# Performance work log

Hardware: AMD Instinct MI355X
Metric: run time of the kernel (lower is better)

The kernel has to match this reference:

```python
import jax, jax.numpy as jnp
import numpy as np

N_NODES = 100000
N_EDGES = 1600000
N_FEAT = 128
N_HID = 128
N_LAYERS = 3
N_GRAPHS = 64
EPS0 = 0.1


def setup_inputs() -> dict:
    key = jax.random.key(0)
    ks = jax.random.split(key, 16)
    x = jax.random.normal(ks[0], (N_NODES, N_FEAT), dtype=jnp.float32)
    edge_index = jax.random.randint(ks[1], (2, N_EDGES), 0, N_NODES, dtype=jnp.int64)
    batch = jnp.sort(jax.random.randint(ks[2], (N_NODES,), 0, N_GRAPHS, dtype=jnp.int64))
    s = 1.0 / np.sqrt(N_HID)
    W_pre1 = jax.random.normal(ks[3], (N_FEAT, N_HID), dtype=jnp.float32) * s
    b_pre1 = jnp.zeros((N_HID,), dtype=jnp.float32)
    W_pre2 = jax.random.normal(ks[4], (N_HID, N_HID), dtype=jnp.float32) * s
    b_pre2 = jnp.zeros((N_HID,), dtype=jnp.float32)
    # stacked per-layer GIN MLP params: Linear -> ReLU -> Linear
    W1s = jax.random.normal(ks[5], (N_LAYERS, N_HID, N_HID), dtype=jnp.float32) * s
    b1s = jnp.zeros((N_LAYERS, N_HID), dtype=jnp.float32)
    W2s = jax.random.normal(ks[6], (N_LAYERS, N_HID, N_HID), dtype=jnp.float32) * s
    b2s = jnp.zeros((N_LAYERS, N_HID), dtype=jnp.float32)
    eps = jnp.full((N_LAYERS,), EPS0, dtype=jnp.float32)
    return {"x": x, "edge_index": edge_index, "batch": batch,
            "W_pre1": W_pre1, "b_pre1": b_pre1, "W_pre2": W_pre2, "b_pre2": b_pre2,
            "W1s": W1s, "b1s": b1s, "W2s": W2s, "b2s": b2s, "eps": eps}


def reference(x, edge_index, batch, W_pre1, b_pre1, W_pre2, b_pre2, W1s, b1s, W2s, b2s, eps):
    n_nodes = x.shape[0]
    src, dst = edge_index[0], edge_index[1]
    # pre-linear stack
    h = jax.nn.relu(x @ W_pre1 + b_pre1)
    h = jax.nn.relu(h @ W_pre2 + b_pre2)
    pooled = []
    for i in range(N_LAYERS):
        # GINConv: sum-aggregate neighbor features (gather from src, scatter-add to dst)
        agg = jax.ops.segment_sum(h[src], dst, num_segments=n_nodes)
        z = (1.0 + eps[i]) * h + agg
        # MLP update: Linear -> ReLU -> Linear
        h = jax.nn.relu(z @ W1s[i] + b1s[i]) @ W2s[i] + b2s[i]
        # global sum pool per graph
        pooled.append(jax.ops.segment_sum(h, batch, num_segments=N_GRAPHS))
    return jnp.concatenate(pooled, axis=1)  # [N_GRAPHS, N_LAYERS * N_HID]
```

## Files before the change

### kernel.cpp

```cpp
#include <hip/hip_runtime.h>

typedef float f32x4 __attribute__((ext_vector_type(4)));
typedef short s16x8 __attribute__((ext_vector_type(8)));

#define ECAP 36864

__device__ __forceinline__ ushort f2bf(float f) {
  uint u = __builtin_bit_cast(uint, f);
  u += 0x7fffu + ((u >> 16) & 1u);
  return (ushort)(u >> 16);
}
__device__ __forceinline__ float bfu_lo(uint u) { return __builtin_bit_cast(float, u << 16); }
__device__ __forceinline__ float bfu_hi(uint u) { return __builtin_bit_cast(float, u & 0xffff0000u); }

__global__ void k_prepw(const float* __restrict__ Wp1, const float* __restrict__ Wp2,
                        const float* __restrict__ W1s, const float* __restrict__ W2s,
                        ushort* __restrict__ Wf, int* __restrict__ bcur, int nbk) {
  int t = blockIdx.x * blockDim.x + threadIdx.x;
  if (t <= nbk) bcur[t] = t * ECAP;
  if (t >= 8 * 2048) return;
  int m = t >> 11;
  int r = t & 2047;
  int lane = r & 63;
  int ksnt = r >> 6;
  int ks = ksnt & 3;
  int nt = ksnt >> 2;
  const float* src = (m == 0) ? Wp1 : (m == 1) ? Wp2
                     : (m < 5) ? (W1s + (size_t)(m - 2) * 16384)
                               : (W2s + (size_t)(m - 5) * 16384);
  ushort* dst = Wf + (size_t)m * 16384 + (size_t)r * 8;
  int c = nt * 16 + (lane & 15);
  int kbase = ks * 32 + (lane >> 4) * 8;
  for (int i = 0; i < 8; ++i) dst[i] = f2bf(src[(size_t)(kbase + i) * 128 + c]);
}

#define PNBK 64
#define PCAP 80
#define PEPB 2048
__global__ __launch_bounds__(256)
void k_part(const int* __restrict__ src, const int* __restrict__ dst,
            int* __restrict__ bcur, uint2* __restrict__ ebuf, int E) {
  __shared__ uint2 stage[PNBK][PCAP];
  __shared__ int lcnt[PNBK];
  int tid = threadIdx.x;
  if (tid < PNBK) lcnt[tid] = 0;
  __syncthreads();
  int e0 = blockIdx.x * PEPB;
  for (int r = 0; r < PEPB / 256; ++r) {
    int e = e0 + r * 256 + tid;
    if (e < E) {
      int d = dst[e], s = src[e];
      int b = d >> 11;
      int pos = atomicAdd(&lcnt[b], 1);
      uint2 pr; pr.x = (uint)s; pr.y = (uint)d;
      if (pos < PCAP) {
        stage[b][pos] = pr;
      } else {
        int p = atomicAdd(&bcur[b], 1);
        ebuf[p] = pr;
      }
    }
    if (r == 3 || r == PEPB / 256 - 1) {
      __syncthreads();
      if (tid < PNBK) {
        int c = lcnt[tid];
        if (c > PCAP) c = PCAP;
        if (c > 0) {
          int base = atomicAdd(&bcur[tid], c);
          for (int i = 0; i < c; ++i) ebuf[base + i] = stage[tid][i];
          lcnt[tid] = 0;
        }
      }
      __syncthreads();
    }
  }
}

__global__ __launch_bounds__(1024)
void k_sort(const uint2* __restrict__ ebuf, const int* __restrict__ bcur,
            int* __restrict__ rowbeg, int* __restrict__ rowend,
            int* __restrict__ csr, int N) {
  __shared__ int lcnt[2048];
  __shared__ int loff[2048];
  __shared__ int wsum[16];
  const int b = blockIdx.x;
  const int tid = threadIdx.x;
  const int lane = tid & 63, w = tid >> 6;
  const int base_e = b * ECAP;
  const int node0 = b << 11;
  const int ecnt = bcur[b] - base_e;

  lcnt[tid] = 0; lcnt[tid + 1024] = 0;
  __syncthreads();
  for (int i = tid; i < ecnt; i += 1024) {
    int d = (int)ebuf[base_e + i].y;
    atomicAdd(&lcnt[d - node0], 1);
  }
  __syncthreads();
  int v0 = lcnt[2 * tid], v1 = lcnt[2 * tid + 1];
  int s = v0 + v1;
  for (int off = 1; off < 64; off <<= 1) {
    int t = __shfl_up(s, off);
    if (lane >= off) s += t;
  }
  if (lane == 63) wsum[w] = s;
  __syncthreads();
  if (w == 0 && lane < 16) {
    int x = wsum[lane];
    int sx = x;
    for (int off = 1; off < 16; off <<= 1) {
      int t = __shfl_up(sx, off);
      if (lane >= off) sx += t;
    }
    wsum[lane] = sx - x;
  }
  __syncthreads();
  int excl = wsum[w] + (s - v0 - v1);
  loff[2 * tid] = excl;
  loff[2 * tid + 1] = excl + v0;
  __syncthreads();
  for (int i = tid; i < 2048; i += 1024) {
    int g = node0 + i;
    if (g < N) {
      int rb = base_e + loff[i];
      rowbeg[g] = rb;
      rowend[g] = rb + lcnt[i];
    }
    lcnt[i] = 0;
  }
  __syncthreads();
  for (int i = tid; i < ecnt; i += 1024) {
    uint2 p = ebuf[base_e + i];
    int dloc = (int)p.y - node0;
    int pos = base_e + loff[dloc] + atomicAdd(&lcnt[dloc], 1);
    csr[pos] = (int)p.x;
  }
}

__global__ __launch_bounds__(256, 8)
void k_layer(const ushort* __restrict__ H, const int* __restrict__ rowbeg,
             const int* __restrict__ rowend, const int* __restrict__ csr,
             const ushort* __restrict__ Wf1, const ushort* __restrict__ Wf2,
             const float* __restrict__ b1, const float* __restrict__ b2,
             const float* __restrict__ eps, int layer,
             ushort* __restrict__ Hout, const int* __restrict__ batch,
             float* __restrict__ pool, int col_off, int M) {
  __shared__ uint Tz[1024];
  __shared__ uint Tt[1024];
  const int tid = threadIdx.x;
  const int w = tid >> 6, lane = tid & 63;
  const int m0 = blockIdx.x * 16;
  const float e = 1.0f + eps[layer];
  const uint* h32 = (const uint*)H;

  for (int r = 0; r < 4; ++r) {
    const int row = w * 4 + r;
    const int n = m0 + row;
    if (n < M) {
      uint u = h32[(size_t)n * 64 + lane];
      float a0 = bfu_lo(u) * e, a1 = bfu_hi(u) * e;
      int s0 = rowbeg[n], s1 = rowend[n];
      for (int base = s0; base < s1; base += 64) {
        int cnt = s1 - base;
        if (cnt > 64) cnt = 64;
        int idx = (lane < cnt) ? csr[base + lane] : 0;
        int j = 0;
        for (; j + 4 <= cnt; j += 4) {
          int i0 = __shfl(idx, j), i1 = __shfl(idx, j + 1);
          int i2 = __shfl(idx, j + 2), i3 = __shfl(idx, j + 3);
          uint u0 = h32[(size_t)i0 * 64 + lane];
          uint u1 = h32[(size_t)i1 * 64 + lane];
          uint u2 = h32[(size_t)i2 * 64 + lane];
          uint u3 = h32[(size_t)i3 * 64 + lane];
          a0 += bfu_lo(u0); a1 += bfu_hi(u0);
          a0 += bfu_lo(u1); a1 += bfu_hi(u1);
          a0 += bfu_lo(u2); a1 += bfu_hi(u2);
          a0 += bfu_lo(u3); a1 += bfu_hi(u3);
        }
        for (; j < cnt; ++j) {
          int si = __shfl(idx, j);
          uint uu = h32[(size_t)si * 64 + lane];
          a0 += bfu_lo(uu); a1 += bfu_hi(uu);
        }
      }
      Tz[row * 64 + (lane ^ ((row & 7) << 2))] = (uint)f2bf(a0) | ((uint)f2bf(a1) << 16);
    }
  }
  __syncthreads();

  const int row16 = lane & 15, hi = lane >> 4;
  const int c2 = w << 1;
  const s16x8* wf1 = (const s16x8*)Wf1;
  f32x4 acc0 = (f32x4){0.f, 0.f, 0.f, 0.f};
  f32x4 acc1 = (f32x4){0.f, 0.f, 0.f, 0.f};
#pragma unroll
  for (int ks = 0; ks < 4; ++ks) {
    const s16x8 af = *(const s16x8*)(Tz + row16 * 64 + ((ks * 16 + hi * 4) ^ ((row16 & 7) << 2)));
    acc0 = __builtin_amdgcn_mfma_f32_16x16x32_bf16(af, wf1[((c2 + 0) * 4 + ks) * 64 + lane], acc0, 0, 0, 0);
    acc1 = __builtin_amdgcn_mfma_f32_16x16x32_bf16(af, wf1[((c2 + 1) * 4 + ks) * 64 + lane], acc1, 0, 0, 0);
  }
  {
    ushort* Tb = (ushort*)Tt;
    const float bb0 = b1[(c2 + 0) * 16 + row16];
    const float bb1 = b1[(c2 + 1) * 16 + row16];
#pragma unroll
    for (int i = 0; i < 4; ++i) {
      const int rr = hi * 4 + i;
      Tb[(rr * 128 + (c2 + 0) * 16 + row16) ^ ((rr & 7) << 3)] = f2bf(fmaxf(acc0[i] + bb0, 0.f));
      Tb[(rr * 128 + (c2 + 1) * 16 + row16) ^ ((rr & 7) << 3)] = f2bf(fmaxf(acc1[i] + bb1, 0.f));
    }
  }
  __syncthreads();

  const s16x8* wf2 = (const s16x8*)Wf2;
  f32x4 ac0 = (f32x4){0.f, 0.f, 0.f, 0.f};
  f32x4 ac1 = (f32x4){0.f, 0.f, 0.f, 0.f};
#pragma unroll
  for (int ks = 0; ks < 4; ++ks) {
    const s16x8 af = *(const s16x8*)(Tt + row16 * 64 + ((ks * 16 + hi * 4) ^ ((row16 & 7) << 2)));
    ac0 = __builtin_amdgcn_mfma_f32_16x16x32_bf16(af, wf2[((c2 + 0) * 4 + ks) * 64 + lane], ac0, 0, 0, 0);
    ac1 = __builtin_amdgcn_mfma_f32_16x16x32_bf16(af, wf2[((c2 + 1) * 4 + ks) * 64 + lane], ac1, 0, 0, 0);
  }
  {
    const int r0 = m0 + hi * 4;
    const int col0 = (c2 + 0) * 16 + row16, col1 = (c2 + 1) * 16 + row16;
    const float bb0 = b2[col0], bb1 = b2[col1];
    const bool full = (m0 + 15 < M);
    const int gf = batch[m0 < M ? m0 : (M - 1)];
    const int gl = batch[(m0 + 15) < M ? (m0 + 15) : (M - 1)];
    if (full && gf == gl) {
      float vs0 = 0.f, vs1 = 0.f;
#pragma unroll
      for (int i = 0; i < 4; ++i) {
        float v0 = ac0[i] + bb0, v1 = ac1[i] + bb1;
        Hout[(size_t)(r0 + i) * 128 + col0] = f2bf(v0);
        Hout[(size_t)(r0 + i) * 128 + col1] = f2bf(v1);
        vs0 += v0; vs1 += v1;
      }
      vs0 += __shfl_xor(vs0, 16); vs0 += __shfl_xor(vs0, 32);
      vs1 += __shfl_xor(vs1, 16); vs1 += __shfl_xor(vs1, 32);
      if (lane < 16) {
        atomicAdd(&pool[(size_t)gf * 384 + col_off + (c2 + 0) * 16 + lane], vs0);
        atomicAdd(&pool[(size_t)gf * 384 + col_off + (c2 + 1) * 16 + lane], vs1);
      }
    } else {
#pragma unroll
      for (int i = 0; i < 4; ++i) {
        const int rr = r0 + i;
        if (rr < M) {
          float v0 = ac0[i] + bb0, v1 = ac1[i] + bb1;
          Hout[(size_t)rr * 128 + col0] = f2bf(v0);
          Hout[(size_t)rr * 128 + col1] = f2bf(v1);
          int g = batch[rr];
          atomicAdd(&pool[(size_t)g * 384 + col_off + col0], v0);
          atomicAdd(&pool[(size_t)g * 384 + col_off + col1], v1);
        }
      }
    }
  }
}

__global__ __launch_bounds__(256, 4)
void k_mlp2(const float* __restrict__ X, const ushort* __restrict__ Wf1,
            const ushort* __restrict__ Wf2, const float* __restrict__ b1,
            const float* __restrict__ b2, ushort* __restrict__ Hout, int M) {
  __shared__ uint lt[4][1024];
  const int lane = threadIdx.x & 63;
  const int wid = threadIdx.x >> 6;
  uint* T = lt[wid];
  const int m0 = blockIdx.x * 64 + wid * 16;
  if (m0 >= M) return;
  const int row = lane & 15, hi = lane >> 4;

  f32x4 acc[8];
#pragma unroll
  for (int nt = 0; nt < 8; ++nt) acc[nt] = (f32x4){0.f, 0.f, 0.f, 0.f};
  {
    const float* xrow = X + (size_t)(m0 + row) * 128;
    const s16x8* wf = (const s16x8*)Wf1;
#pragma unroll
    for (int ks = 0; ks < 4; ++ks) {
      float4 xa = *(const float4*)&xrow[ks * 32 + hi * 8];
      float4 xb = *(const float4*)&xrow[ks * 32 + hi * 8 + 4];
      s16x8 af;
      af[0] = (short)f2bf(xa.x); af[1] = (short)f2bf(xa.y);
      af[2] = (short)f2bf(xa.z); af[3] = (short)f2bf(xa.w);
      af[4] = (short)f2bf(xb.x); af[5] = (short)f2bf(xb.y);
      af[6] = (short)f2bf(xb.z); af[7] = (short)f2bf(xb.w);
#pragma unroll
      for (int nt = 0; nt < 8; ++nt)
        acc[nt] = __builtin_amdgcn_mfma_f32_16x16x32_bf16(af, wf[(nt * 4 + ks) * 64 + lane], acc[nt], 0, 0, 0);
    }
  }
  {
    ushort* Tb = (ushort*)T;
    const int r0l = hi * 4;
#pragma unroll
    for (int nt = 0; nt < 8; ++nt) {
      float bb = b1[nt * 16 + row];
      const int col = nt * 16 + row;
#pragma unroll
      for (int i = 0; i < 4; ++i) {
        int lr = r0l + i;
        float v = fmaxf(acc[nt][i] + bb, 0.f);
        Tb[(lr * 128 + col) ^ ((lr & 7) << 3)] = f2bf(v);
      }
    }
  }
#pragma unroll
  for (int nt = 0; nt < 8; ++nt) acc[nt] = (f32x4){0.f, 0.f, 0.f, 0.f};
  {
#pragma unroll
    for (int ks = 0; ks < 4; ++ks) {
      int ub = row * 64 + ((ks * 16 + hi * 4) ^ ((row & 7) << 2));
      s16x8 af = *(const s16x8*)(T + ub);
#pragma unroll
      for (int nt = 0; nt < 8; ++nt)
        acc[nt] = __builtin_amdgcn_mfma_f32_16x16x32_bf16(af, ((const s16x8*)Wf2)[(nt * 4 + ks) * 64 + lane], acc[nt], 0, 0, 0);
    }
  }
  {
    const int r0 = m0 + hi * 4;
#pragma unroll
    for (int nt = 0; nt < 8; ++nt) {
      const int col = nt * 16 + row;
      float bb = b2[col];
#pragma unroll
      for (int i = 0; i < 4; ++i) {
        float v = fmaxf(acc[nt][i] + bb, 0.f);
        Hout[(size_t)(r0 + i) * 128 + col] = f2bf(v);
      }
    }
  }
}

extern "C" void kernel_launch(void* const* d_in, const int* in_sizes, int n_in,
                              void* d_out, int out_size, void* d_ws, size_t ws_size,
                              hipStream_t stream) {
  const float* x    = (const float*)d_in[0];
  const int*   ei   = (const int*)d_in[1];
  const int*   batch= (const int*)d_in[2];
  const float* Wp1  = (const float*)d_in[3];
  const float* bp1  = (const float*)d_in[4];
  const float* Wp2  = (const float*)d_in[5];
  const float* bp2  = (const float*)d_in[6];
  const float* W1s  = (const float*)d_in[7];
  const float* b1s  = (const float*)d_in[8];
  const float* W2s  = (const float*)d_in[9];
  const float* b2s  = (const float*)d_in[10];
  const float* eps  = (const float*)d_in[11];

  const int N = in_sizes[0] / 128;
  const int E = in_sizes[1] / 2;
  float* out = (float*)d_out;
  const int nbk = (N + 2047) >> 11;

  char* ws = (char*)d_ws;
  size_t off = 0;
  auto alloc = [&](size_t bytes) -> void* {
    void* p = ws + off;
    off += (bytes + 255) & ~(size_t)255;
    return p;
  };
  ushort* bufA  = (ushort*)alloc((size_t)N * 128 * 2);
  ushort* bufB  = (ushort*)alloc((size_t)N * 128 * 2);
  ushort* Wf    = (ushort*)alloc((size_t)8 * 16384 * 2);
  int* rowbeg   = (int*)alloc((size_t)N * 4);
  int* rowend   = (int*)alloc((size_t)N * 4);
  int* csr      = (int*)alloc((size_t)nbk * ECAP * 4);
  uint2* ebuf   = (uint2*)alloc((size_t)nbk * ECAP * 8);
  int* bcur     = (int*)alloc((size_t)(nbk + 1) * 4);
  (void)ws_size; (void)n_in;

  hipMemsetAsync(out, 0, (size_t)out_size * 4, stream);

  k_prepw<<<64, 256, 0, stream>>>(Wp1, Wp2, W1s, W2s, Wf, bcur, nbk);
  k_part<<<(E + PEPB - 1) / PEPB, 256, 0, stream>>>(ei, ei + E, bcur, ebuf, E);
  k_sort<<<nbk, 1024, 0, stream>>>(ebuf, bcur, rowbeg, rowend, csr, N);

  const int ngrid = (N + 63) / 64;
  k_mlp2<<<ngrid, 256, 0, stream>>>(x, Wf + 0 * 16384, Wf + 1 * 16384, bp1, bp2, bufA, N);

  const int lgrid = (N + 15) / 16;
  ushort* hin = bufA;
  ushort* hout = bufB;
  for (int L = 0; L < 3; ++L) {
    k_layer<<<lgrid, 256, 0, stream>>>(hin, rowbeg, rowend, csr,
                                       Wf + (2 + L) * 16384, Wf + (5 + L) * 16384,
                                       b1s + (size_t)L * 128, b2s + (size_t)L * 128,
                                       eps, L, hout, batch, out, L * 128, N);
    ushort* tmp = hin; hin = hout; hout = tmp;
  }
}
```

Before: 362.5 us.

## Warp-specialize GIN layer kernel: gather warps overlap with MLP warp via double buffer

The layer kernel becomes persistent with 384 threads: five warps gather and aggregate neighbour features for the next 16-row tile into one shared buffer, while a sixth warp runs the full two-layer MLP on the previous tile from the other buffer. This is meant to hide the MFMA/MLP phase behind the memory-bound gather and drop the extra barrier between the MLP stages. In exchange, a single warp now does all MLP work for a tile, which could become the bottleneck. The grid is also capped at 1280 blocks.

After: 1.358 ms. +274.7%, slower.

```diff
diff --git a/kernel.cpp b/kernel.cpp
--- a/kernel.cpp
+++ b/kernel.cpp
@@ -137,7 +137,87 @@
   }
 }
 
-__global__ __launch_bounds__(256, 8)
+__device__ __forceinline__ void mlp_tile(uint* T, int m0,
+    const s16x8* __restrict__ wf1, const s16x8* __restrict__ wf2,
+    const float* __restrict__ b1, const float* __restrict__ b2,
+    ushort* __restrict__ Hout, const int* __restrict__ batch,
+    float* __restrict__ pool, int col_off, int M, int lane) {
+  const int row = lane & 15, hi = lane >> 4;
+  f32x4 acc[8];
+#pragma unroll
+  for (int nt = 0; nt < 8; ++nt) acc[nt] = (f32x4){0.f, 0.f, 0.f, 0.f};
+#pragma unroll
+  for (int ks = 0; ks < 4; ++ks) {
+    const s16x8 af = *(const s16x8*)(T + row * 64 + ((ks * 16 + hi * 4) ^ ((row & 7) << 2)));
+#pragma unroll
+    for (int nt = 0; nt < 8; ++nt)
+      acc[nt] = __builtin_amdgcn_mfma_f32_16x16x32_bf16(af, wf1[(nt * 4 + ks) * 64 + lane], acc[nt], 0, 0, 0);
+  }
+  {
+    ushort* Tb = (ushort*)T;
+#pragma unroll
+    for (int nt = 0; nt < 8; ++nt) {
+      float bb = b1[nt * 16 + row];
+      const int col = nt * 16 + row;
+#pragma unroll
+      for (int i = 0; i < 4; ++i) {
+        int lr = hi * 4 + i;
+        float v = fmaxf(acc[nt][i] + bb, 0.f);
+        Tb[(lr * 128 + col) ^ ((lr & 7) << 3)] = f2bf(v);
+      }
+    }
+  }
+#pragma unroll
+  for (int nt = 0; nt < 8; ++nt) acc[nt] = (f32x4){0.f, 0.f, 0.f, 0.f};
+#pragma unroll
+  for (int ks = 0; ks < 4; ++ks) {
+    const s16x8 af = *(const s16x8*)(T + row * 64 + ((ks * 16 + hi * 4) ^ ((row & 7) << 2)));
+#pragma unroll
+    for (int nt = 0; nt < 8; ++nt)
+      acc[nt] = __builtin_amdgcn_mfma_f32_16x16x32_bf16(af, wf2[(nt * 4 + ks) * 64 + lane], acc[nt], 0, 0, 0);
+  }
+  {
+    const int r0 = m0 + hi * 4;
+    const bool full = (m0 + 15 < M);
+    const int gf = batch[m0 < M ? m0 : (M - 1)];
+    const int gl = batch[(m0 + 15) < M ? (m0 + 15) : (M - 1)];
+    if (full && gf == gl) {
+#pragma unroll
+      for (int nt = 0; nt < 8; ++nt) {
+        const int col = nt * 16 + row;
+        float bb = b2[col];
+        float vs = 0.f;
+#pragma unroll
+        for (int i = 0; i < 4; ++i) {
+          float v = acc[nt][i] + bb;
+          Hout[(size_t)(r0 + i) * 128 + col] = f2bf(v);
+          vs += v;
+        }
+        vs += __shfl_xor(vs, 16);
+        vs += __shfl_xor(vs, 32);
+        if (lane < 16) atomicAdd(&pool[(size_t)gf * 384 + col_off + nt * 16 + lane], vs);
+      }
+    } else {
+#pragma unroll
+      for (int nt = 0; nt < 8; ++nt) {
+        const int col = nt * 16 + row;
+        float bb = b2[col];
+#pragma unroll
+        for (int i = 0; i < 4; ++i) {
+          const int rr = r0 + i;
+          if (rr < M) {
+            float v = acc[nt][i] + bb;
+            Hout[(size_t)rr * 128 + col] = f2bf(v);
+            int g = batch[rr];
+            atomicAdd(&pool[(size_t)g * 384 + col_off + col], v);
+          }
+        }
+      }
+    }
+  }
+}
+
+__global__ __launch_bounds__(384, 7)
 void k_layer(const ushort* __restrict__ H, const int* __restrict__ rowbeg,
              const int* __restrict__ rowend, const int* __restrict__ csr,
              const ushort* __restrict__ Wf1, const ushort* __restrict__ Wf2,
@@ -145,119 +225,63 @@
              const float* __restrict__ eps, int layer,
              ushort* __restrict__ Hout, const int* __restrict__ batch,
              float* __restrict__ pool, int col_off, int M) {
-  __shared__ uint Tz[1024];
-  __shared__ uint Tt[1024];
+  __shared__ uint Tz[2][1024];
   const int tid = threadIdx.x;
   const int w = tid >> 6, lane = tid & 63;
-  const int m0 = blockIdx.x * 16;
   const float e = 1.0f + eps[layer];
   const uint* h32 = (const uint*)H;
-
-  for (int r = 0; r < 4; ++r) {
-    const int row = w * 4 + r;
-    const int n = m0 + row;
-    if (n < M) {
-      uint u = h32[(size_t)n * 64 + lane];
-      float a0 = bfu_lo(u) * e, a1 = bfu_hi(u) * e;
-      int s0 = rowbeg[n], s1 = rowend[n];
-      for (int base = s0; base < s1; base += 64) {
-        int cnt = s1 - base;
-        if (cnt > 64) cnt = 64;
-        int idx = (lane < cnt) ? csr[base + lane] : 0;
-        int j = 0;
-        for (; j + 4 <= cnt; j += 4) {
-          int i0 = __shfl(idx, j), i1 = __shfl(idx, j + 1);
-          int i2 = __shfl(idx, j + 2), i3 = __shfl(idx, j + 3);
-          uint u0 = h32[(size_t)i0 * 64 + lane];
-          uint u1 = h32[(size_t)i1 * 64 + lane];
-          uint u2 = h32[(size_t)i2 * 64 + lane];
-          uint u3 = h32[(size_t)i3 * 64 + lane];
-          a0 += bfu_lo(u0); a1 += bfu_hi(u0);
-          a0 += bfu_lo(u1); a1 += bfu_hi(u1);
-          a0 += bfu_lo(u2); a1 += bfu_hi(u2);
-          a0 += bfu_lo(u3); a1 += bfu_hi(u3);
+  const s16x8* wf1 = (const s16x8*)Wf1;
+  const s16x8* wf2 = (const s16x8*)Wf2;
+  const int ntiles = (M + 15) >> 4;
+
+  int prev = -1;
+  int buf = 0;
+  for (int t = blockIdx.x; t < ntiles; t += gridDim.x) {
+    if (w < 5) {
+      const int rs = (w * 16) / 5;
+      const int re = ((w + 1) * 16) / 5;
+      uint* T = Tz[buf];
+      for (int row = rs; row < re; ++row) {
+        const int n = t * 16 + row;
+        if (n < M) {
+          uint u = h32[(size_t)n * 64 + lane];
+          float a0 = bfu_lo(u) * e, a1 = bfu_hi(u) * e;
+          int s0 = rowbeg[n], s1 = rowend[n];
+          for (int base = s0; base < s1; base += 64) {
+            int cnt = s1 - base;
+            if (cnt > 64) cnt = 64;
+            int idx = (lane < cnt) ? csr[base + lane] : 0;
+            int j = 0;
+            for (; j + 4 <= cnt; j += 4) {
+              int i0 = __shfl(idx, j), i1 = __shfl(idx, j + 1);
+              int i2 = __shfl(idx, j + 2), i3 = __shfl(idx, j + 3);
+              uint u0 = h32[(size_t)i0 * 64 + lane];
+              uint u1 = h32[(size_t)i1 * 64 + lane];
+              uint u2 = h32[(size_t)i2 * 64 + lane];
+              uint u3 = h32[(size_t)i3 * 64 + lane];
+              a0 += bfu_lo(u0); a1 += bfu_hi(u0);
+              a0 += bfu_lo(u1); a1 += bfu_hi(u1);
+              a0 += bfu_lo(u2); a1 += bfu_hi(u2);
+              a0 += bfu_lo(u3); a1 += bfu_hi(u3);
+            }
+            for (; j < cnt; ++j) {
+              int si = __shfl(idx, j);
+              uint uu = h32[(size_t)si * 64 + lane];
+              a0 += bfu_lo(uu); a1 += bfu_hi(uu);
+            }
+          }
+          T[row * 64 + (lane ^ ((row & 7) << 2))] = (uint)f2bf(a0) | ((uint)f2bf(a1) << 16);
         }
-        for (; j < cnt; ++j) {
-          int si = __shfl(idx, j);
-          uint uu = h32[(size_t)si * 64 + lane];
-          a0 += bfu_lo(uu); a1 += bfu_hi(uu);
-        }
-      }
-      Tz[row * 64 + (lane ^ ((row & 7) << 2))] = (uint)f2bf(a0) | ((uint)f2bf(a1) << 16);
-    }
-  }
-  __syncthreads();
-
-  const int row16 = lane & 15, hi = lane >> 4;
-  const int c2 = w << 1;
-  const s16x8* wf1 = (const s16x8*)Wf1;
-  f32x4 acc0 = (f32x4){0.f, 0.f, 0.f, 0.f};
-  f32x4 acc1 = (f32x4){0.f, 0.f, 0.f, 0.f};
-#pragma unroll
-  for (int ks = 0; ks < 4; ++ks) {
-    const s16x8 af = *(const s16x8*)(Tz + row16 * 64 + ((ks * 16 + hi * 4) ^ ((row16 & 7) << 2)));
-    acc0 = __builtin_amdgcn_mfma_f32_16x16x32_bf16(af, wf1[((c2 + 0) * 4 + ks) * 64 + lane], acc0, 0, 0, 0);
-    acc1 = __builtin_amdgcn_mfma_f32_16x16x32_bf16(af, wf1[((c2 + 1) * 4 + ks) * 64 + lane], acc1, 0, 0, 0);
-  }
-  {
-    ushort* Tb = (ushort*)Tt;
-    const float bb0 = b1[(c2 + 0) * 16 + row16];
-    const float bb1 = b1[(c2 + 1) * 16 + row16];
-#pragma unroll
-    for (int i = 0; i < 4; ++i) {
-      const int rr = hi * 4 + i;
-      Tb[(rr * 128 + (c2 + 0) * 16 + row16) ^ ((rr & 7) << 3)] = f2bf(fmaxf(acc0[i] + bb0, 0.f));
-      Tb[(rr * 128 + (c2 + 1) * 16 + row16) ^ ((rr & 7) << 3)] = f2bf(fmaxf(acc1[i] + bb1, 0.f));
-    }
-  }
-  __syncthreads();
-
-  const s16x8* wf2 = (const s16x8*)Wf2;
-  f32x4 ac0 = (f32x4){0.f, 0.f, 0.f, 0.f};
-  f32x4 ac1 = (f32x4){0.f, 0.f, 0.f, 0.f};
-#pragma unroll
-  for (int ks = 0; ks < 4; ++ks) {
-    const s16x8 af = *(const s16x8*)(Tt + row16 * 64 + ((ks * 16 + hi * 4) ^ ((row16 & 7) << 2)));
-    ac0 = __builtin_amdgcn_mfma_f32_16x16x32_bf16(af, wf2[((c2 + 0) * 4 + ks) * 64 + lane], ac0, 0, 0, 0);
-    ac1 = __builtin_amdgcn_mfma_f32_16x16x32_bf16(af, wf2[((c2 + 1) * 4 + ks) * 64 + lane], ac1, 0, 0, 0);
-  }
-  {
-    const int r0 = m0 + hi * 4;
-    const int col0 = (c2 + 0) * 16 + row16, col1 = (c2 + 1) * 16 + row16;
-    const float bb0 = b2[col0], bb1 = b2[col1];
-    const bool full = (m0 + 15 < M);
-    const int gf = batch[m0 < M ? m0 : (M - 1)];
-    const int gl = batch[(m0 + 15) < M ? (m0 + 15) : (M - 1)];
-    if (full && gf == gl) {
-      float vs0 = 0.f, vs1 = 0.f;
-#pragma unroll
-      for (int i = 0; i < 4; ++i) {
-        float v0 = ac0[i] + bb0, v1 = ac1[i] + bb1;
-        Hout[(size_t)(r0 + i) * 128 + col0] = f2bf(v0);
-        Hout[(size_t)(r0 + i) * 128 + col1] = f2bf(v1);
-        vs0 += v0; vs1 += v1;
-      }
-      vs0 += __shfl_xor(vs0, 16); vs0 += __shfl_xor(vs0, 32);
-      vs1 += __shfl_xor(vs1, 16); vs1 += __shfl_xor(vs1, 32);
-      if (lane < 16) {
-        atomicAdd(&pool[(size_t)gf * 384 + col_off + (c2 + 0) * 16 + lane], vs0);
-        atomicAdd(&pool[(size_t)gf * 384 + col_off + (c2 + 1) * 16 + lane], vs1);
-      }
-    } else {
-#pragma unroll
-      for (int i = 0; i < 4; ++i) {
-        const int rr = r0 + i;
-        if (rr < M) {
-          float v0 = ac0[i] + bb0, v1 = ac1[i] + bb1;
-          Hout[(size_t)rr * 128 + col0] = f2bf(v0);
-          Hout[(size_t)rr * 128 + col1] = f2bf(v1);
-          int g = batch[rr];
-          atomicAdd(&pool[(size_t)g * 384 + col_off + col0], v0);
-          atomicAdd(&pool[(size_t)g * 384 + col_off + col1], v1);
-        }
-      }
-    }
-  }
+      }
+    } else if (prev >= 0) {
+      mlp_tile(Tz[buf ^ 1], prev * 16, wf1, wf2, b1, b2, Hout, batch, pool, col_off, M, lane);
+    }
+    __syncthreads();
+    prev = t;
+    buf ^= 1;
+  }
+  if (w == 5 && prev >= 0)
+    mlp_tile(Tz[buf ^ 1], prev * 16, wf1, wf2, b1, b2, Hout, batch, pool, col_off, M, lane);
 }
 
 __global__ __launch_bounds__(256, 4)
@@ -381,11 +405,13 @@
   const int ngrid = (N + 63) / 64;
   k_mlp2<<<ngrid, 256, 0, stream>>>(x, Wf + 0 * 16384, Wf + 1 * 16384, bp1, bp2, bufA, N);
 
-  const int lgrid = (N + 15) / 16;
+  const int ntiles = (N + 15) / 16;
+  int lgrid = 256 * 5;
+  if (lgrid > ntiles) lgrid = ntiles;
   ushort* hin = bufA;
   ushort* hout = bufB;
   for (int L = 0; L < 3; ++L) {
-    k_layer<<<lgrid, 256, 0, stream>>>(hin, rowbeg, rowend, csr,
+    k_layer<<<lgrid, 384, 0, stream>>>(hin, rowbeg, rowend, csr,
                                        Wf + (2 + L) * 16384, Wf + (5 + L) * 16384,
                                        b1s + (size_t)L * 128, b2s + (size_t)L * 128,
                                        eps, L, hout, batch, out, L * 128, N);
```

## Pack edge pairs into one word, enlarge staging, fold output memset

Applied to the files above, without the earlier changes.

Edges in the partition buffer are now packed into a single 32-bit word (source shifted left 11 bits, ORed with the local destination index), which halves ebuf traffic in both the partition and sort kernels. The shared staging capacity per bucket grows from 80 to 128 entries, so fewer edges overflow into direct global atomics. The separate output memset is dropped and the weight-prep kernel zeroes the output instead, saving one launch. Packing assumes source indices fit in 21 bits (up to about 2M nodes).

After: 351.4 us. 3.1% less time.

```diff
diff --git a/kernel.cpp b/kernel.cpp
--- a/kernel.cpp
+++ b/kernel.cpp
@@ -15,9 +15,11 @@
 
 __global__ void k_prepw(const float* __restrict__ Wp1, const float* __restrict__ Wp2,
                         const float* __restrict__ W1s, const float* __restrict__ W2s,
-                        ushort* __restrict__ Wf, int* __restrict__ bcur, int nbk) {
+                        ushort* __restrict__ Wf, int* __restrict__ bcur, int nbk,
+                        float* __restrict__ out, int out_size) {
   int t = blockIdx.x * blockDim.x + threadIdx.x;
   if (t <= nbk) bcur[t] = t * ECAP;
+  for (int i = t; i < out_size; i += 16384) out[i] = 0.f;
   if (t >= 8 * 2048) return;
   int m = t >> 11;
   int r = t & 2047;
@@ -35,12 +37,12 @@
 }
 
 #define PNBK 64
-#define PCAP 80
+#define PCAP 128
 #define PEPB 2048
 __global__ __launch_bounds__(256)
 void k_part(const int* __restrict__ src, const int* __restrict__ dst,
-            int* __restrict__ bcur, uint2* __restrict__ ebuf, int E) {
-  __shared__ uint2 stage[PNBK][PCAP];
+            int* __restrict__ bcur, uint* __restrict__ ebuf, int E) {
+  __shared__ uint stage[PNBK][PCAP];
   __shared__ int lcnt[PNBK];
   int tid = threadIdx.x;
   if (tid < PNBK) lcnt[tid] = 0;
@@ -51,13 +53,13 @@
     if (e < E) {
       int d = dst[e], s = src[e];
       int b = d >> 11;
+      uint pk = ((uint)s << 11) | (uint)(d & 2047);
       int pos = atomicAdd(&lcnt[b], 1);
-      uint2 pr; pr.x = (uint)s; pr.y = (uint)d;
       if (pos < PCAP) {
-        stage[b][pos] = pr;
+        stage[b][pos] = pk;
       } else {
         int p = atomicAdd(&bcur[b], 1);
-        ebuf[p] = pr;
+        ebuf[p] = pk;
       }
     }
     if (r == 3 || r == PEPB / 256 - 1) {
@@ -77,7 +79,7 @@
 }
 
 __global__ __launch_bounds__(1024)
-void k_sort(const uint2* __restrict__ ebuf, const int* __restrict__ bcur,
+void k_sort(const uint* __restrict__ ebuf, const int* __restrict__ bcur,
             int* __restrict__ rowbeg, int* __restrict__ rowend,
             int* __restrict__ csr, int N) {
   __shared__ int lcnt[2048];
@@ -93,8 +95,8 @@
   lcnt[tid] = 0; lcnt[tid + 1024] = 0;
   __syncthreads();
   for (int i = tid; i < ecnt; i += 1024) {
-    int d = (int)ebuf[base_e + i].y;
-    atomicAdd(&lcnt[d - node0], 1);
+    int dloc = (int)(ebuf[base_e + i] & 2047u);
+    atomicAdd(&lcnt[dloc], 1);
   }
   __syncthreads();
   int v0 = lcnt[2 * tid], v1 = lcnt[2 * tid + 1];
@@ -130,10 +132,10 @@
   }
   __syncthreads();
   for (int i = tid; i < ecnt; i += 1024) {
-    uint2 p = ebuf[base_e + i];
-    int dloc = (int)p.y - node0;
+    uint p = ebuf[base_e + i];
+    int dloc = (int)(p & 2047u);
     int pos = base_e + loff[dloc] + atomicAdd(&lcnt[dloc], 1);
-    csr[pos] = (int)p.x;
+    csr[pos] = (int)(p >> 11);
   }
 }
 
@@ -368,13 +370,11 @@
   int* rowbeg   = (int*)alloc((size_t)N * 4);
   int* rowend   = (int*)alloc((size_t)N * 4);
   int* csr      = (int*)alloc((size_t)nbk * ECAP * 4);
-  uint2* ebuf   = (uint2*)alloc((size_t)nbk * ECAP * 8);
+  uint* ebuf    = (uint*)alloc((size_t)nbk * ECAP * 4);
   int* bcur     = (int*)alloc((size_t)(nbk + 1) * 4);
   (void)ws_size; (void)n_in;
 
-  hipMemsetAsync(out, 0, (size_t)out_size * 4, stream);
-
-  k_prepw<<<64, 256, 0, stream>>>(Wp1, Wp2, W1s, W2s, Wf, bcur, nbk);
+  k_prepw<<<64, 256, 0, stream>>>(Wp1, Wp2, W1s, W2s, Wf, bcur, nbk, out, out_size);
   k_part<<<(E + PEPB - 1) / PEPB, 256, 0, stream>>>(ei, ei + E, bcur, ebuf, E);
   k_sort<<<nbk, 1024, 0, stream>>>(ebuf, bcur, rowbeg, rowend, csr, N);
 
```
